# Optimization experiments

Hardware: AMD Instinct MI355X
Metric: run time of the kernel (lower is better)

## Reference

```python
import jax, jax.numpy as jnp
import numpy as np

N = 50000      # nodes
E = 400000     # edges (avg degree 8)
G = 64         # graphs in batch
IN_DIM = 128
OUT_DIM = 16


def _linear_params(key, fan_in, fan_out):
    k1, k2 = jax.random.split(key)
    s = 1.0 / np.sqrt(fan_in)
    W = jax.random.uniform(k1, (fan_in, fan_out), minval=-s, maxval=s, dtype=jnp.float32)
    b = jax.random.uniform(k2, (fan_out,), minval=-s, maxval=s, dtype=jnp.float32)
    return W, b


def setup_inputs() -> dict:
    key = jax.random.key(0)
    ks = jax.random.split(key, 12)
    x = jax.random.normal(ks[0], (N, IN_DIM), dtype=jnp.float32)
    edge_index = jax.random.randint(ks[1], (2, E), 0, N)
    # balanced graph assignment (sorted, every graph id present)
    batch = (jnp.arange(N) * G) // N
    W1, b1 = _linear_params(ks[2], IN_DIM, 64)
    W2, b2 = _linear_params(ks[3], 64, 256)
    W3, b3 = _linear_params(ks[4], 256, 512)
    W4, b4 = _linear_params(ks[5], 512, 64)
    Wr, br = _linear_params(ks[6], IN_DIM, 64)
    fc1_W, fc1_b = _linear_params(ks[7], 64, 64)
    fc2_W, fc2_b = _linear_params(ks[8], 64, OUT_DIM)
    ln_g = jnp.ones((64,), jnp.float32); ln_b = jnp.zeros((64,), jnp.float32)
    fcn_g = jnp.ones((64,), jnp.float32); fcn_b = jnp.zeros((64,), jnp.float32)
    return dict(x=x, edge_index=edge_index, batch=batch,
                W1=W1, b1=b1, W2=W2, b2=b2, W3=W3, b3=b3, W4=W4, b4=b4,
                Wr=Wr, br=br, ln_g=ln_g, ln_b=ln_b,
                fc1_W=fc1_W, fc1_b=fc1_b, fcn_g=fcn_g, fcn_b=fcn_b,
                fc2_W=fc2_W, fc2_b=fc2_b)


def _leaky_relu(h):
    return jnp.where(h >= 0, h, 0.01 * h)


def _layer_norm(h, g, b, eps=1e-5):
    m = jnp.mean(h, axis=-1, keepdims=True)
    v = jnp.var(h, axis=-1, keepdims=True)
    return (h - m) * jax.lax.rsqrt(v + eps) * g + b


def reference(x, edge_index, batch, W1, b1, W2, b2, W3, b3, W4, b4,
              Wr, br, ln_g, ln_b, fc1_W, fc1_b, fcn_g, fcn_b, fc2_W, fc2_b):
    src, dst = edge_index[0], edge_index[1]
    n = x.shape[0]
    # PyG GCNConv normalization with self-loops: deg = 1 + in-degree
    deg = jax.ops.segment_sum(jnp.ones(src.shape[0], x.dtype), dst, num_segments=n) + 1.0
    dis = jax.lax.rsqrt(deg)                 # [N]
    edge_norm = (dis[src] * dis[dst])[:, None]   # [E,1]
    self_norm = (dis * dis)[:, None]             # [N,1]

    def gcn_conv(h, W, b):
        h = h @ W                                            # transform first (PyG order)
        agg = jax.ops.segment_sum(h[src] * edge_norm, dst, num_segments=n)
        return agg + h * self_norm + b                       # self-loop term + bias

    residual = x @ Wr + br
    h = _leaky_relu(gcn_conv(x, W1, b1))
    h = _leaky_relu(gcn_conv(h, W2, b2))
    h = _leaky_relu(gcn_conv(h, W3, b3))
    h = _leaky_relu(gcn_conv(h, W4, b4))
    h = _layer_norm(h + residual, ln_g, ln_b)
    # global max pool over graphs
    p = jax.ops.segment_max(h, batch, num_segments=G)        # [G,64]
    p = _layer_norm(p @ fc1_W + fc1_b, fcn_g, fcn_b)
    p = _leaky_relu(p)
    return p @ fc2_W + fc2_b                                 # [G,16]
```

## Files before the change

kernel.cpp:

```cpp
#include <hip/hip_runtime.h>
#include <hip/hip_bf16.h>
#include <math.h>

typedef short bf16x8 __attribute__((ext_vector_type(8)));
typedef short bf16x4 __attribute__((ext_vector_type(4)));
typedef float f32x4 __attribute__((ext_vector_type(4)));

__device__ inline unsigned short f2bf(float f) {
  unsigned u = __float_as_uint(f);
  u += 0x7FFF + ((u >> 16) & 1);
  return (unsigned short)(u >> 16);
}
__device__ inline float bf2f(unsigned short h) {
  return __uint_as_float(((unsigned)h) << 16);
}


__global__ __launch_bounds__(256) void zero_i32(int* __restrict__ p, int n) {
  int i = blockIdx.x * 256 + threadIdx.x;
  if (i < n) p[i] = 0;
}

__global__ __launch_bounds__(256) void count_k(const int* __restrict__ dst, int* __restrict__ cnt, int e) {
  int i = blockIdx.x * 256 + threadIdx.x;
  if (i < e) atomicAdd(&cnt[dst[i]], 1);
}

__global__ __launch_bounds__(256) void dis_k(const int* __restrict__ cnt, float* __restrict__ dis, int n) {
  int i = blockIdx.x * 256 + threadIdx.x;
  if (i < n) dis[i] = rsqrtf((float)cnt[i] + 1.0f);
}

__global__ __launch_bounds__(256) void scan_a(const int* __restrict__ cnt, int* __restrict__ bsum, int n) {
  int i = blockIdx.x * 256 + threadIdx.x;
  int v = (i < n) ? cnt[i] : 0;
#pragma unroll
  for (int o = 32; o > 0; o >>= 1) v += __shfl_xor(v, o);
  __shared__ int ws[4];
  if ((threadIdx.x & 63) == 0) ws[threadIdx.x >> 6] = v;
  __syncthreads();
  if (threadIdx.x == 0) bsum[blockIdx.x] = ws[0] + ws[1] + ws[2] + ws[3];
}

__global__ __launch_bounds__(256) void scan_b(const int* __restrict__ bsum, int* __restrict__ bpre,
                                              int* __restrict__ off_n, int nb) {
  __shared__ int s[256];
  int t = threadIdx.x;
  int v = (t < nb) ? bsum[t] : 0;
  s[t] = v;
  __syncthreads();
  for (int o = 1; o < 256; o <<= 1) {
    int u = (t >= o) ? s[t - o] : 0;
    __syncthreads();
    s[t] += u;
    __syncthreads();
  }
  if (t < nb) bpre[t] = s[t] - v;
  if (t == 255) off_n[0] = s[255];
}

__global__ __launch_bounds__(256) void scan_c(const int* __restrict__ cnt, const int* __restrict__ bpre,
                                              int* __restrict__ off, int* __restrict__ cursor, int n) {
  __shared__ int s[256];
  int i = blockIdx.x * 256 + threadIdx.x;
  int t = threadIdx.x;
  int v = (i < n) ? cnt[i] : 0;
  s[t] = v;
  __syncthreads();
  for (int o = 1; o < 256; o <<= 1) {
    int u = (t >= o) ? s[t - o] : 0;
    __syncthreads();
    s[t] += u;
    __syncthreads();
  }
  if (i < n) {
    int ov = bpre[blockIdx.x] + s[t] - v;
    off[i] = ov;
    cursor[i] = ov;
  }
}

__global__ __launch_bounds__(256) void scatter_k(const int* __restrict__ src, const int* __restrict__ dst,
                                                 int* __restrict__ cursor, int* __restrict__ csr, int e) {
  int i = blockIdx.x * 256 + threadIdx.x;
  if (i < e) {
    int p = atomicAdd(&cursor[dst[i]], 1);
    csr[p] = src[i];
  }
}


__global__ __launch_bounds__(256) void wconv_k(const float* __restrict__ W1, const float* __restrict__ Wr,
                                               const float* __restrict__ W2, const float* __restrict__ W3,
                                               const float* __restrict__ W4,
                                               short* __restrict__ o1, short* __restrict__ oR,
                                               short* __restrict__ o2, short* __restrict__ o3,
                                               short* __restrict__ o4) {
  int b = blockIdx.x;
  const float* W; short* O; int K, N, nr;
  if (b < 64)       { W = W1; O = o1; K = 128; N = 64;  nr = b; }
  else if (b < 128) { W = Wr; O = oR; K = 128; N = 64;  nr = b - 64; }
  else if (b < 384) { W = W2; O = o2; K = 64;  N = 256; nr = b - 128; }
  else if (b < 896) { W = W3; O = o3; K = 256; N = 512; nr = b - 384; }
  else              { W = W4; O = o4; K = 512; N = 64;  nr = b - 896; }
  for (int k = threadIdx.x; k < K; k += 256)
    O[(size_t)nr * K + k] = (short)f2bf(W[(size_t)k * N + nr]);
}


template<int KT, int NTOT, int WM, int WN, int BIAS, int RELU, int ABF, int OBF, int SPLIT, int SCL, int BLK>
__global__ __launch_bounds__(256, BLK) void mgemm(const void* __restrict__ Av,
                                                  const short* __restrict__ Wc,
                                                  const float* __restrict__ bias,
                                                  void* __restrict__ Cv, void* __restrict__ Cv2,
                                                  const float* __restrict__ scl, int M) {
  __shared__ short As[64 * WM][ABF ? 40 : 72];
  __shared__ short Bs[64 * WN][40];
  const int tid = threadIdx.x;
  const int row0 = blockIdx.x * (64 * WM);
  const int col0 = blockIdx.y * (64 * WN);
  const int w = tid >> 6, lane = tid & 63;
  const int wm = w / WN, wn = w % WN;
  const int rm = wm * 64, cn = wn * 64;
  const int lm = lane & 15, lk = (lane >> 4) * 8;

  f32x4 acc[4][4];
#pragma unroll
  for (int i = 0; i < 4; i++)
#pragma unroll
    for (int j = 0; j < 4; j++)
#pragma unroll
      for (int r = 0; r < 4; r++) acc[i][j][r] = 0.f;

  for (int k0 = 0; k0 < KT; k0 += 32) {
#pragma unroll
    for (int p = 0; p < WM; p++) {
      int r = (tid >> 2) + p * 64;
      int kseg = (tid & 3) * 8;
      int gr = row0 + r;
      if (ABF) {
        bf16x8 v = {0, 0, 0, 0, 0, 0, 0, 0};
        if (gr < M) v = *(const bf16x8*)((const short*)Av + (size_t)gr * KT + k0 + kseg);
        *(bf16x8*)&As[r][kseg] = v;
      } else {
        float4 v0 = {0.f, 0.f, 0.f, 0.f}, v1 = {0.f, 0.f, 0.f, 0.f};
        if (gr < M) {
          const float* ap = (const float*)Av + (size_t)gr * KT + k0 + kseg;
          v0 = *(const float4*)ap;
          v1 = *(const float4*)(ap + 4);
        }
        float vv[8] = {v0.x, v0.y, v0.z, v0.w, v1.x, v1.y, v1.z, v1.w};
        bf16x8 hv, lv;
#pragma unroll
        for (int j = 0; j < 8; j++) {
          unsigned short h = f2bf(vv[j]);
          hv[j] = (short)h;
          lv[j] = (short)f2bf(vv[j] - bf2f(h));
        }
        *(bf16x8*)&As[r][kseg] = hv;
        *(bf16x8*)&As[r][32 + kseg] = lv;
      }
    }
#pragma unroll
    for (int p = 0; p < WN; p++) {
      int nr = (tid >> 2) + p * 64;
      int seg = (tid & 3) * 8;
      *(bf16x8*)&Bs[nr][seg] = *(const bf16x8*)(Wc + (size_t)(col0 + nr) * KT + k0 + seg);
    }
    __syncthreads();

    bf16x8 ah[4], al[4], bb[4];
#pragma unroll
    for (int mt = 0; mt < 4; mt++) {
      ah[mt] = *(const bf16x8*)&As[rm + mt * 16 + lm][lk];
      if (!ABF) al[mt] = *(const bf16x8*)&As[rm + mt * 16 + lm][32 + lk];
    }
#pragma unroll
    for (int nt = 0; nt < 4; nt++) bb[nt] = *(const bf16x8*)&Bs[cn + nt * 16 + lm][lk];
#pragma unroll
    for (int mt = 0; mt < 4; mt++)
#pragma unroll
      for (int nt = 0; nt < 4; nt++) {
        acc[mt][nt] = __builtin_amdgcn_mfma_f32_16x16x32_bf16(ah[mt], bb[nt], acc[mt][nt], 0, 0, 0);
        if (!ABF)
          acc[mt][nt] = __builtin_amdgcn_mfma_f32_16x16x32_bf16(al[mt], bb[nt], acc[mt][nt], 0, 0, 0);
      }
    __syncthreads();
  }

  if (SPLIT) {
    short* epi = (short*)&As[0][0];
    if (wn == 0) {
#pragma unroll
      for (int mt = 0; mt < 4; mt++) {
        int lr = rm + mt * 16 + (lane >> 4) * 4;
#pragma unroll
        for (int r = 0; r < 4; r++) {
          int gr = row0 + lr + r;
          float sc = (SCL && gr < M) ? scl[gr] : 0.f;
#pragma unroll
          for (int nt = 0; nt < 4; nt++)
            epi[(lr + r) * 64 + nt * 16 + lm] = (short)f2bf(acc[mt][nt][r] * sc);
        }
      }
    } else {
#pragma unroll
      for (int mt = 0; mt < 4; mt++) {
        int grb = row0 + rm + mt * 16 + (lane >> 4) * 4;
#pragma unroll
        for (int nt = 0; nt < 4; nt++) {
          int gc = nt * 16 + lm;
          float bv = bias[gc];
#pragma unroll
          for (int r = 0; r < 4; r++) {
            int gr = grb + r;
            if (gr < M) ((float*)Cv2)[(size_t)gr * 64 + gc] = acc[mt][nt][r] + bv;
          }
        }
      }
    }
    __syncthreads();
    int base = tid * 32;
    int row = base >> 6, col = base & 63;
    int gr = row0 + row;
    if (gr < M) {
#pragma unroll
      for (int q = 0; q < 4; q++)
        *(bf16x8*)((short*)Cv + (size_t)gr * 64 + col + q * 8) = *(bf16x8*)&epi[base + q * 8];
    }
  } else if (OBF && WM == 1) {
    short* epi = &Bs[0][0];
    const int NCOL = 64 * WN;
    float bvv[4];
#pragma unroll
    for (int nt = 0; nt < 4; nt++) bvv[nt] = BIAS ? bias[col0 + cn + nt * 16 + lm] : 0.f;
#pragma unroll
    for (int mt = 0; mt < 4; mt++) {
      __syncthreads();
#pragma unroll
      for (int r = 0; r < 4; r++) {
        int gr = row0 + mt * 16 + (lane >> 4) * 4 + r;
        float sc = (SCL && gr < M) ? scl[gr] : 1.f;
#pragma unroll
        for (int nt = 0; nt < 4; nt++) {
          float v = acc[mt][nt][r] + bvv[nt];
          if (RELU) v = (v >= 0.f) ? v : 0.01f * v;
          if (SCL) v *= sc;
          epi[((lane >> 4) * 4 + r) * NCOL + cn + nt * 16 + lm] = (short)f2bf(v);
        }
      }
      __syncthreads();
      const int per = (16 * NCOL) / 256;
      int base = tid * per;
      int lr = base / NCOL, lc = base % NCOL;
      int gr = row0 + mt * 16 + lr;
      if (gr < M) {
#pragma unroll
        for (int q = 0; q < per / 8; q++)
          *(bf16x8*)((short*)Cv + (size_t)gr * NTOT + col0 + lc + q * 8) = *(bf16x8*)&epi[base + q * 8];
      }
    }
  } else {
#pragma unroll
    for (int mt = 0; mt < 4; mt++) {
      int grb = row0 + rm + mt * 16 + (lane >> 4) * 4;
#pragma unroll
      for (int nt = 0; nt < 4; nt++) {
        int gc = col0 + cn + nt * 16 + lm;
        float bv = BIAS ? bias[gc] : 0.f;
#pragma unroll
        for (int r = 0; r < 4; r++) {
          int gr = grb + r;
          if (gr < M) {
            float v = acc[mt][nt][r] + bv;
            if (RELU) v = (v >= 0.f) ? v : 0.01f * v;
            if (SCL) v *= scl[gr];
            if (OBF) ((short*)Cv)[(size_t)gr * NTOT + gc] = (short)f2bf(v);
            else     ((float*)Cv)[(size_t)gr * NTOT + gc] = v;
          }
        }
      }
    }
  }
}


__global__ __launch_bounds__(256, 5) void fused34_k(const short* __restrict__ z3,
                                                    const short* __restrict__ W3c,
                                                    const float* __restrict__ b3,
                                                    const short* __restrict__ W4c,
                                                    const float* __restrict__ dis,
                                                    float* __restrict__ T4, int M) {
  __shared__ short Bs[32][264];
  __shared__ short Hs[64][40];
  __shared__ short Ws4[64][40];
  const int tid = threadIdx.x;
  const int row0 = blockIdx.x * 64;
  const int w = tid >> 6, lane = tid & 63;
  const int lm = lane & 15, lk = (lane >> 4) * 8;
  const int rquad = (lane >> 4) * 4;

  bf16x8 afr[8];
  {
    int gr = row0 + w * 16 + lm;
    bool ok = gr < M;
    const short* zp = z3 + (size_t)gr * 256 + lk;
#pragma unroll
    for (int kc = 0; kc < 8; kc++) {
      bf16x8 v = {0, 0, 0, 0, 0, 0, 0, 0};
      if (ok) v = *(const bf16x8*)(zp + kc * 32);
      afr[kc] = v;
    }
  }

  f32x4 t4acc[4];
#pragma unroll
  for (int nt = 0; nt < 4; nt++)
#pragma unroll
    for (int r = 0; r < 4; r++) t4acc[nt][r] = 0.f;

  for (int c = 0; c < 16; c++) {
#pragma unroll
    for (int q = 0; q < 4; q++) {
      int flat = q * 2048 + tid * 8;
      int rr = flat >> 8, cc = flat & 255;
      *(bf16x8*)&Bs[rr][cc] = *(const bf16x8*)(W3c + (size_t)c * 32 * 256 + flat);
    }
    Ws4[tid >> 2][(tid & 3) * 8 + 0] = 0;
    *(bf16x8*)&Ws4[tid >> 2][(tid & 3) * 8] =
        *(const bf16x8*)(W4c + (size_t)(tid >> 2) * 512 + c * 32 + (tid & 3) * 8);
    __syncthreads();

    f32x4 acc1[2];
#pragma unroll
    for (int nt = 0; nt < 2; nt++)
#pragma unroll
      for (int r = 0; r < 4; r++) acc1[nt][r] = 0.f;
#pragma unroll
    for (int k0 = 0; k0 < 8; k0++) {
      bf16x8 bb[2];
#pragma unroll
      for (int nt = 0; nt < 2; nt++) bb[nt] = *(const bf16x8*)&Bs[nt * 16 + lm][k0 * 32 + lk];
#pragma unroll
      for (int nt = 0; nt < 2; nt++)
        acc1[nt] = __builtin_amdgcn_mfma_f32_16x16x32_bf16(afr[k0], bb[nt], acc1[nt], 0, 0, 0);
    }
#pragma unroll
    for (int nt = 0; nt < 2; nt++) {
      float bv = b3[c * 32 + nt * 16 + lm];
#pragma unroll
      for (int r = 0; r < 4; r++) {
        float v = acc1[nt][r] + bv;
        v = (v >= 0.f) ? v : 0.01f * v;
        Hs[w * 16 + rquad + r][nt * 16 + lm] = (short)f2bf(v);
      }
    }
    {
      bf16x8 ah2 = *(const bf16x8*)&Hs[w * 16 + lm][lk];
      bf16x8 bb2[4];
#pragma unroll
      for (int nt = 0; nt < 4; nt++) bb2[nt] = *(const bf16x8*)&Ws4[nt * 16 + lm][lk];
#pragma unroll
      for (int nt = 0; nt < 4; nt++)
        t4acc[nt] = __builtin_amdgcn_mfma_f32_16x16x32_bf16(ah2, bb2[nt], t4acc[nt], 0, 0, 0);
    }
    __syncthreads();
  }
#pragma unroll
  for (int r = 0; r < 4; r++) {
    int gr = row0 + w * 16 + rquad + r;
    float sc = (gr < M) ? dis[gr] : 0.f;
#pragma unroll
    for (int nt = 0; nt < 4; nt++) {
      int gc = nt * 16 + lm;
      if (gr < M) T4[(size_t)gr * 64 + gc] = t4acc[nt][r] * sc;
    }
  }
}


template<int BR, int OSCL>
__global__ __launch_bounds__(256) void aggb64_k(const short* __restrict__ T, const float* __restrict__ dis,
                                                const int* __restrict__ off, const int* __restrict__ csr,
                                                const float* __restrict__ bias, short* __restrict__ Out, int n) {
  int wid = (blockIdx.x * 256 + threadIdx.x) >> 6;
  int lane = threadIdx.x & 63;
  if (wid >= n) return;
  float di = dis[wid];
  int e0 = off[wid], e1 = off[wid + 1];
  float acc = bf2f((unsigned short)T[(size_t)wid * 64 + lane]);
  int e = e0;
  for (; e + 4 <= e1; e += 4) {
    int j0 = csr[e], j1 = csr[e + 1], j2 = csr[e + 2], j3 = csr[e + 3];
    float v0 = bf2f((unsigned short)T[(size_t)j0 * 64 + lane]);
    float v1 = bf2f((unsigned short)T[(size_t)j1 * 64 + lane]);
    float v2 = bf2f((unsigned short)T[(size_t)j2 * 64 + lane]);
    float v3 = bf2f((unsigned short)T[(size_t)j3 * 64 + lane]);
    acc += (v0 + v1) + (v2 + v3);
  }
  for (; e < e1; e++) acc += bf2f((unsigned short)T[(size_t)csr[e] * 64 + lane]);
  float v = di * acc;
  if (BR) {
    v += bias[lane];
    v = (v >= 0.f) ? v : 0.01f * v;
  }
  if (OSCL) v *= di;
  Out[(size_t)wid * 64 + lane] = (short)f2bf(v);
}

__global__ __launch_bounds__(256) void agg64_ln_k(const float* __restrict__ T, const float* __restrict__ dis,
                                                  const int* __restrict__ off, const int* __restrict__ csr,
                                                  const float* __restrict__ bias, const float* __restrict__ resid,
                                                  const float* __restrict__ g, const float* __restrict__ b,
                                                  float* __restrict__ outh, int n) {
  int wid = (blockIdx.x * 256 + threadIdx.x) >> 6;
  int lane = threadIdx.x & 63;
  if (wid >= n) return;
  float di = dis[wid];
  int e0 = off[wid], e1 = off[wid + 1];
  float acc = T[(size_t)wid * 64 + lane];
  int e = e0;
  for (; e + 4 <= e1; e += 4) {
    int j0 = csr[e], j1 = csr[e + 1], j2 = csr[e + 2], j3 = csr[e + 3];
    float v0 = T[(size_t)j0 * 64 + lane];
    float v1 = T[(size_t)j1 * 64 + lane];
    float v2 = T[(size_t)j2 * 64 + lane];
    float v3 = T[(size_t)j3 * 64 + lane];
    acc += (v0 + v1) + (v2 + v3);
  }
  for (; e < e1; e++) acc += T[(size_t)csr[e] * 64 + lane];
  float v = di * acc + bias[lane];
  v = (v >= 0.f) ? v : 0.01f * v;
  v += resid[(size_t)wid * 64 + lane];
  float s = v, ss = v * v;
#pragma unroll
  for (int o = 32; o > 0; o >>= 1) {
    s += __shfl_xor(s, o);
    ss += __shfl_xor(ss, o);
  }
  float m = s * (1.f / 64.f);
  float var = ss * (1.f / 64.f) - m * m;
  float y = (v - m) * rsqrtf(var + 1e-5f) * g[lane] + b[lane];
  outh[(size_t)wid * 64 + lane] = y;
}

__global__ __launch_bounds__(256) void agg256b_k(const short* __restrict__ T, const float* __restrict__ dis,
                                                 const int* __restrict__ off, const int* __restrict__ csr,
                                                 short* __restrict__ Out, int n) {
  int wid = (blockIdx.x * 256 + threadIdx.x) >> 6;
  int lane = threadIdx.x & 63;
  if (wid >= n) return;
  float di = dis[wid];
  int e0 = off[wid], e1 = off[wid + 1];
  bf16x4 sf = *(const bf16x4*)&T[(size_t)wid * 256 + lane * 4];
  float a0 = bf2f((unsigned short)sf[0]);
  float a1 = bf2f((unsigned short)sf[1]);
  float a2 = bf2f((unsigned short)sf[2]);
  float a3 = bf2f((unsigned short)sf[3]);
  int e = e0;
  for (; e + 4 <= e1; e += 4) {
    int j0 = csr[e], j1 = csr[e + 1], j2 = csr[e + 2], j3 = csr[e + 3];
    bf16x4 t0 = *(const bf16x4*)&T[(size_t)j0 * 256 + lane * 4];
    bf16x4 t1 = *(const bf16x4*)&T[(size_t)j1 * 256 + lane * 4];
    bf16x4 t2 = *(const bf16x4*)&T[(size_t)j2 * 256 + lane * 4];
    bf16x4 t3 = *(const bf16x4*)&T[(size_t)j3 * 256 + lane * 4];
    a0 += (bf2f((unsigned short)t0[0]) + bf2f((unsigned short)t1[0])) +
          (bf2f((unsigned short)t2[0]) + bf2f((unsigned short)t3[0]));
    a1 += (bf2f((unsigned short)t0[1]) + bf2f((unsigned short)t1[1])) +
          (bf2f((unsigned short)t2[1]) + bf2f((unsigned short)t3[1]));
    a2 += (bf2f((unsigned short)t0[2]) + bf2f((unsigned short)t1[2])) +
          (bf2f((unsigned short)t2[2]) + bf2f((unsigned short)t3[2]));
    a3 += (bf2f((unsigned short)t0[3]) + bf2f((unsigned short)t1[3])) +
          (bf2f((unsigned short)t2[3]) + bf2f((unsigned short)t3[3]));
  }
  for (; e < e1; e++) {
    bf16x4 t = *(const bf16x4*)&T[(size_t)csr[e] * 256 + lane * 4];
    a0 += bf2f((unsigned short)t[0]);
    a1 += bf2f((unsigned short)t[1]);
    a2 += bf2f((unsigned short)t[2]);
    a3 += bf2f((unsigned short)t[3]);
  }
  bf16x4 o;
  o[0] = (short)f2bf(di * a0);
  o[1] = (short)f2bf(di * a1);
  o[2] = (short)f2bf(di * a2);
  o[3] = (short)f2bf(di * a3);
  *(bf16x4*)&Out[(size_t)wid * 256 + lane * 4] = o;
}


__global__ __launch_bounds__(256) void pool_k(const float* __restrict__ hn, float* __restrict__ p, int n) {
  const int G = 64;
  int g = blockIdx.x;
  int f = threadIdx.x & 63, c = threadIdx.x >> 6;
  long long s = ((long long)g * n + G - 1) / G;
  long long e = ((long long)(g + 1) * n + G - 1) / G;
  float m = -INFINITY;
  for (long long i = s + c; i < e; i += 4) m = fmaxf(m, hn[(size_t)i * 64 + f]);
  __shared__ float red[4][64];
  red[c][f] = m;
  __syncthreads();
  if (c == 0) {
    m = fmaxf(fmaxf(red[0][f], red[1][f]), fmaxf(red[2][f], red[3][f]));
    p[g * 64 + f] = m;
  }
}


__global__ __launch_bounds__(64) void mlp_k(const float* __restrict__ p, const float* __restrict__ fc1W,
                                            const float* __restrict__ fc1b, const float* __restrict__ fng,
                                            const float* __restrict__ fnb, const float* __restrict__ fc2W,
                                            const float* __restrict__ fc2b, float* __restrict__ out) {
  int g = blockIdx.x;
  int lane = threadIdx.x;
  __shared__ float ps[64], qs[64];
  ps[lane] = p[g * 64 + lane];
  __syncthreads();
  float q = fc1b[lane];
#pragma unroll 8
  for (int k = 0; k < 64; k++) q = fmaf(ps[k], fc1W[k * 64 + lane], q);
  float s = q, ss = q * q;
#pragma unroll
  for (int o = 32; o > 0; o >>= 1) {
    s += __shfl_xor(s, o);
    ss += __shfl_xor(ss, o);
  }
  float m = s * (1.f / 64.f);
  float var = ss * (1.f / 64.f) - m * m;
  float y = (q - m) * rsqrtf(var + 1e-5f) * fng[lane] + fnb[lane];
  y = (y >= 0.f) ? y : 0.01f * y;
  qs[lane] = y;
  __syncthreads();
  if (lane < 16) {
    float o = fc2b[lane];
#pragma unroll 8
    for (int k = 0; k < 64; k++) o = fmaf(qs[k], fc2W[k * 16 + lane], o);
    out[g * 16 + lane] = o;
  }
}


extern "C" void kernel_launch(void* const* d_in, const int* in_sizes, int n_in,
                              void* d_out, int out_size, void* d_ws, size_t ws_size,
                              hipStream_t stream) {
  const float* x   = (const float*)d_in[0];
  const int*   ei  = (const int*)d_in[1];
  const float* W1  = (const float*)d_in[3];
  const float* b1  = (const float*)d_in[4];
  const float* W2  = (const float*)d_in[5];
  const float* b2  = (const float*)d_in[6];
  const float* W3  = (const float*)d_in[7];
  const float* b3  = (const float*)d_in[8];
  const float* W4  = (const float*)d_in[9];
  const float* b4  = (const float*)d_in[10];
  const float* Wr  = (const float*)d_in[11];
  const float* br  = (const float*)d_in[12];
  const float* lng = (const float*)d_in[13];
  const float* lnb = (const float*)d_in[14];
  const float* f1W = (const float*)d_in[15];
  const float* f1b = (const float*)d_in[16];
  const float* fng = (const float*)d_in[17];
  const float* fnb = (const float*)d_in[18];
  const float* f2W = (const float*)d_in[19];
  const float* f2b = (const float*)d_in[20];

  int n = in_sizes[0] / 128;
  int e = in_sizes[1] / 2;
  const int* src = ei;
  const int* dst = ei + e;

  float* arena = (float*)d_ws;
  float* resid = arena;
  short* h2b   = (short*)(arena + (size_t)64 * n);
  float* t4    = arena + (size_t)64 * n;
  short* z3b   = (short*)(arena + (size_t)192 * n);
  float* hn    = arena + (size_t)192 * n;
  short* t1b   = (short*)(arena + (size_t)320 * n);
  short* h1b   = (short*)(arena + (size_t)352 * n);
  short* z2b   = (short*)(arena + (size_t)384 * n);
  float* dis   = arena + (size_t)448 * n;
  int* cnt    = (int*)(dis + n);
  int* off    = cnt + n;
  int* cursor = off + n + 1;
  int* csr    = cursor + n;
  int* bsum   = csr + e;
  int* bpre   = bsum + 256;
  float* pool = (float*)(bpre + 256);
  size_t wq = (((size_t)(pool + 4096)) + 15) & ~(size_t)15;
  short* wc1 = (short*)wq;
  short* wcR = wc1 + 8192;
  short* wc2 = wcR + 8192;
  short* wc3 = wc2 + 16384;
  short* wc4 = wc3 + 131072;
  size_t need = ((char*)(wc4 + 32768) - (char*)d_ws) + 64;
  if (ws_size < need) return;

  int nb_n = (n + 255) / 256;
  int nb_e = (e + 255) / 256;
  int nb_w = (n + 3) / 4;
  int g_wide = (n + 63) / 64;
  int g_fused = (n + 127) / 128;

  wconv_k<<<960, 256, 0, stream>>>(W1, Wr, W2, W3, W4, wc1, wcR, wc2, wc3, wc4);

  zero_i32<<<nb_n, 256, 0, stream>>>(cnt, n);
  count_k<<<nb_e, 256, 0, stream>>>(dst, cnt, e);
  dis_k<<<nb_n, 256, 0, stream>>>(cnt, dis, n);
  scan_a<<<nb_n, 256, 0, stream>>>(cnt, bsum, n);
  scan_b<<<1, 256, 0, stream>>>(bsum, bpre, off + n, nb_n);
  scan_c<<<nb_n, 256, 0, stream>>>(cnt, bpre, off, cursor, n);
  scatter_k<<<nb_e, 256, 0, stream>>>(src, dst, cursor, csr, e);

  mgemm<128, 128, 2, 2, 1, 0, 0, 0, 1, 1, 4><<<dim3(g_fused, 1), 256, 0, stream>>>(x, wc1, br, t1b, resid, dis, n);
  aggb64_k<1, 1><<<nb_w, 256, 0, stream>>>(t1b, dis, off, csr, b1, h1b, n);
  aggb64_k<0, 0><<<nb_w, 256, 0, stream>>>(h1b, dis, off, csr, nullptr, z2b, n);
  mgemm<64, 256, 1, 4, 1, 1, 1, 1, 0, 1, 5><<<dim3(g_wide, 1), 256, 0, stream>>>(z2b, wc2, b2, h2b, nullptr, dis, n);
  agg256b_k<<<nb_w, 256, 0, stream>>>(h2b, dis, off, csr, z3b, n);
  fused34_k<<<g_wide, 256, 0, stream>>>(z3b, wc3, b3, wc4, dis, t4, n);
  agg64_ln_k<<<nb_w, 256, 0, stream>>>(t4, dis, off, csr, b4, resid, lng, lnb, hn, n);
  pool_k<<<64, 256, 0, stream>>>(hn, pool, n);
  mlp_k<<<64, 64, 0, stream>>>(pool, f1W, f1b, fng, fnb, f2W, f2b, (float*)d_out);
}
```

Before: 387.9 us.

## Double-buffer fused34 weights, unroll gathers by 8, fuse small kernels

The fused layer-3/4 kernel now double-buffers its W3/W4 tiles in shared memory. It prefetches the next chunk into registers while computing the current one, which removes one barrier per iteration, and occupancy is lowered to 3 blocks to allow for the larger LDS use. The CSR aggregation kernels gain an 8-way unrolled gather loop to keep more loads in flight. The degree-normalisation kernel is folded into scan_c, and pool and MLP are merged into one kernel, removing two launches. The costs are higher register and LDS pressure and lower occupancy in fused34.

```diff
diff --git a/kernel.cpp b/kernel.cpp
--- a/kernel.cpp
+++ b/kernel.cpp
@@ -24,11 +24,6 @@
 __global__ __launch_bounds__(256) void count_k(const int* __restrict__ dst, int* __restrict__ cnt, int e) {
   int i = blockIdx.x * 256 + threadIdx.x;
   if (i < e) atomicAdd(&cnt[dst[i]], 1);
-}
-
-__global__ __launch_bounds__(256) void dis_k(const int* __restrict__ cnt, float* __restrict__ dis, int n) {
-  int i = blockIdx.x * 256 + threadIdx.x;
-  if (i < n) dis[i] = rsqrtf((float)cnt[i] + 1.0f);
 }
 
 __global__ __launch_bounds__(256) void scan_a(const int* __restrict__ cnt, int* __restrict__ bsum, int n) {
@@ -60,7 +55,8 @@
 }
 
 __global__ __launch_bounds__(256) void scan_c(const int* __restrict__ cnt, const int* __restrict__ bpre,
-                                              int* __restrict__ off, int* __restrict__ cursor, int n) {
+                                              int* __restrict__ off, int* __restrict__ cursor,
+                                              float* __restrict__ dis, int n) {
   __shared__ int s[256];
   int i = blockIdx.x * 256 + threadIdx.x;
   int t = threadIdx.x;
@@ -77,6 +73,7 @@
     int ov = bpre[blockIdx.x] + s[t] - v;
     off[i] = ov;
     cursor[i] = ov;
+    dis[i] = rsqrtf((float)v + 1.0f);
   }
 }
 
@@ -285,20 +282,22 @@
 }
 
 
-__global__ __launch_bounds__(256, 5) void fused34_k(const short* __restrict__ z3,
+__global__ __launch_bounds__(256, 3) void fused34_k(const short* __restrict__ z3,
                                                     const short* __restrict__ W3c,
                                                     const float* __restrict__ b3,
                                                     const short* __restrict__ W4c,
                                                     const float* __restrict__ dis,
                                                     float* __restrict__ T4, int M) {
-  __shared__ short Bs[32][264];
+  __shared__ short Bs[2][32][264];
+  __shared__ short Ws4[2][64][40];
   __shared__ short Hs[64][40];
-  __shared__ short Ws4[64][40];
   const int tid = threadIdx.x;
   const int row0 = blockIdx.x * 64;
   const int w = tid >> 6, lane = tid & 63;
   const int lm = lane & 15, lk = (lane >> 4) * 8;
   const int rquad = (lane >> 4) * 4;
+  const int w3row = tid >> 5, w3seg = (tid & 31) * 8;
+  const int w4row = tid >> 2, w4seg = (tid & 3) * 8;
 
   bf16x8 afr[8];
   {
@@ -319,17 +318,32 @@
 #pragma unroll
     for (int r = 0; r < 4; r++) t4acc[nt][r] = 0.f;
 
+  bf16x8 pw3[4];
+  bf16x8 pw4;
+#pragma unroll
+  for (int q = 0; q < 4; q++) {
+    int flat = q * 2048 + tid * 8;
+    pw3[q] = *(const bf16x8*)(W3c + flat);
+  }
+  pw4 = *(const bf16x8*)(W4c + (size_t)w4row * 512 + w4seg);
+#pragma unroll
+  for (int q = 0; q < 4; q++) {
+    int flat = q * 2048 + tid * 8;
+    *(bf16x8*)&Bs[0][flat >> 8][flat & 255] = pw3[q];
+  }
+  *(bf16x8*)&Ws4[0][w4row][w4seg] = pw4;
+  __syncthreads();
+
   for (int c = 0; c < 16; c++) {
-#pragma unroll
-    for (int q = 0; q < 4; q++) {
-      int flat = q * 2048 + tid * 8;
-      int rr = flat >> 8, cc = flat & 255;
-      *(bf16x8*)&Bs[rr][cc] = *(const bf16x8*)(W3c + (size_t)c * 32 * 256 + flat);
-    }
-    Ws4[tid >> 2][(tid & 3) * 8 + 0] = 0;
-    *(bf16x8*)&Ws4[tid >> 2][(tid & 3) * 8] =
-        *(const bf16x8*)(W4c + (size_t)(tid >> 2) * 512 + c * 32 + (tid & 3) * 8);
-    __syncthreads();
+    int cur = c & 1, nxt = cur ^ 1;
+    if (c < 15) {
+#pragma unroll
+      for (int q = 0; q < 4; q++) {
+        int flat = q * 2048 + tid * 8;
+        pw3[q] = *(const bf16x8*)(W3c + (size_t)(c + 1) * 32 * 256 + flat);
+      }
+      pw4 = *(const bf16x8*)(W4c + (size_t)w4row * 512 + (c + 1) * 32 + w4seg);
+    }
 
     f32x4 acc1[2];
 #pragma unroll
@@ -340,7 +354,7 @@
     for (int k0 = 0; k0 < 8; k0++) {
       bf16x8 bb[2];
 #pragma unroll
-      for (int nt = 0; nt < 2; nt++) bb[nt] = *(const bf16x8*)&Bs[nt * 16 + lm][k0 * 32 + lk];
+      for (int nt = 0; nt < 2; nt++) bb[nt] = *(const bf16x8*)&Bs[cur][nt * 16 + lm][k0 * 32 + lk];
 #pragma unroll
       for (int nt = 0; nt < 2; nt++)
         acc1[nt] = __builtin_amdgcn_mfma_f32_16x16x32_bf16(afr[k0], bb[nt], acc1[nt], 0, 0, 0);
@@ -359,10 +373,18 @@
       bf16x8 ah2 = *(const bf16x8*)&Hs[w * 16 + lm][lk];
       bf16x8 bb2[4];
 #pragma unroll
-      for (int nt = 0; nt < 4; nt++) bb2[nt] = *(const bf16x8*)&Ws4[nt * 16 + lm][lk];
+      for (int nt = 0; nt < 4; nt++) bb2[nt] = *(const bf16x8*)&Ws4[cur][nt * 16 + lm][lk];
 #pragma unroll
       for (int nt = 0; nt < 4; nt++)
         t4acc[nt] = __builtin_amdgcn_mfma_f32_16x16x32_bf16(ah2, bb2[nt], t4acc[nt], 0, 0, 0);
+    }
+    if (c < 15) {
+#pragma unroll
+      for (int q = 0; q < 4; q++) {
+        int flat = q * 2048 + tid * 8;
+        *(bf16x8*)&Bs[nxt][flat >> 8][flat & 255] = pw3[q];
+      }
+      *(bf16x8*)&Ws4[nxt][w4row][w4seg] = pw4;
     }
     __syncthreads();
   }
@@ -390,6 +412,19 @@
   int e0 = off[wid], e1 = off[wid + 1];
   float acc = bf2f((unsigned short)T[(size_t)wid * 64 + lane]);
   int e = e0;
+  for (; e + 8 <= e1; e += 8) {
+    int j0 = csr[e], j1 = csr[e + 1], j2 = csr[e + 2], j3 = csr[e + 3];
+    int j4 = csr[e + 4], j5 = csr[e + 5], j6 = csr[e + 6], j7 = csr[e + 7];
+    float v0 = bf2f((unsigned short)T[(size_t)j0 * 64 + lane]);
+    float v1 = bf2f((unsigned short)T[(size_t)j1 * 64 + lane]);
+    float v2 = bf2f((unsigned short)T[(size_t)j2 * 64 + lane]);
+    float v3 = bf2f((unsigned short)T[(size_t)j3 * 64 + lane]);
+    float v4 = bf2f((unsigned short)T[(size_t)j4 * 64 + lane]);
+    float v5 = bf2f((unsigned short)T[(size_t)j5 * 64 + lane]);
+    float v6 = bf2f((unsigned short)T[(size_t)j6 * 64 + lane]);
+    float v7 = bf2f((unsigned short)T[(size_t)j7 * 64 + lane]);
+    acc += ((v0 + v1) + (v2 + v3)) + ((v4 + v5) + (v6 + v7));
+  }
   for (; e + 4 <= e1; e += 4) {
     int j0 = csr[e], j1 = csr[e + 1], j2 = csr[e + 2], j3 = csr[e + 3];
     float v0 = bf2f((unsigned short)T[(size_t)j0 * 64 + lane]);
@@ -420,6 +455,19 @@
   int e0 = off[wid], e1 = off[wid + 1];
   float acc = T[(size_t)wid * 64 + lane];
   int e = e0;
+  for (; e + 8 <= e1; e += 8) {
+    int j0 = csr[e], j1 = csr[e + 1], j2 = csr[e + 2], j3 = csr[e + 3];
+    int j4 = csr[e + 4], j5 = csr[e + 5], j6 = csr[e + 6], j7 = csr[e + 7];
+    float v0 = T[(size_t)j0 * 64 + lane];
+    float v1 = T[(size_t)j1 * 64 + lane];
+    float v2 = T[(size_t)j2 * 64 + lane];
+    float v3 = T[(size_t)j3 * 64 + lane];
+    float v4 = T[(size_t)j4 * 64 + lane];
+    float v5 = T[(size_t)j5 * 64 + lane];
+    float v6 = T[(size_t)j6 * 64 + lane];
+    float v7 = T[(size_t)j7 * 64 + lane];
+    acc += ((v0 + v1) + (v2 + v3)) + ((v4 + v5) + (v6 + v7));
+  }
   for (; e + 4 <= e1; e += 4) {
     int j0 = csr[e], j1 = csr[e + 1], j2 = csr[e + 2], j3 = csr[e + 3];
     float v0 = T[(size_t)j0 * 64 + lane];
@@ -458,20 +506,29 @@
   float a2 = bf2f((unsigned short)sf[2]);
   float a3 = bf2f((unsigned short)sf[3]);
   int e = e0;
+  for (; e + 8 <= e1; e += 8) {
+    bf16x4 t[8];
+#pragma unroll
+    for (int q = 0; q < 8; q++) t[q] = *(const bf16x4*)&T[(size_t)csr[e + q] * 256 + lane * 4];
+#pragma unroll
+    for (int q = 0; q < 8; q++) {
+      a0 += bf2f((unsigned short)t[q][0]);
+      a1 += bf2f((unsigned short)t[q][1]);
+      a2 += bf2f((unsigned short)t[q][2]);
+      a3 += bf2f((unsigned short)t[q][3]);
+    }
+  }
   for (; e + 4 <= e1; e += 4) {
-    int j0 = csr[e], j1 = csr[e + 1], j2 = csr[e + 2], j3 = csr[e + 3];
-    bf16x4 t0 = *(const bf16x4*)&T[(size_t)j0 * 256 + lane * 4];
-    bf16x4 t1 = *(const bf16x4*)&T[(size_t)j1 * 256 + lane * 4];
-    bf16x4 t2 = *(const bf16x4*)&T[(size_t)j2 * 256 + lane * 4];
-    bf16x4 t3 = *(const bf16x4*)&T[(size_t)j3 * 256 + lane * 4];
-    a0 += (bf2f((unsigned short)t0[0]) + bf2f((unsigned short)t1[0])) +
-          (bf2f((unsigned short)t2[0]) + bf2f((unsigned short)t3[0]));
-    a1 += (bf2f((unsigned short)t0[1]) + bf2f((unsigned short)t1[1])) +
-          (bf2f((unsigned short)t2[1]) + bf2f((unsigned short)t3[1]));
-    a2 += (bf2f((unsigned short)t0[2]) + bf2f((unsigned short)t1[2])) +
-          (bf2f((unsigned short)t2[2]) + bf2f((unsigned short)t3[2]));
-    a3 += (bf2f((unsigned short)t0[3]) + bf2f((unsigned short)t1[3])) +
-          (bf2f((unsigned short)t2[3]) + bf2f((unsigned short)t3[3]));
+    bf16x4 t[4];
+#pragma unroll
+    for (int q = 0; q < 4; q++) t[q] = *(const bf16x4*)&T[(size_t)csr[e + q] * 256 + lane * 4];
+#pragma unroll
+    for (int q = 0; q < 4; q++) {
+      a0 += bf2f((unsigned short)t[q][0]);
+      a1 += bf2f((unsigned short)t[q][1]);
+      a2 += bf2f((unsigned short)t[q][2]);
+      a3 += bf2f((unsigned short)t[q][3]);
+    }
   }
   for (; e < e1; e++) {
     bf16x4 t = *(const bf16x4*)&T[(size_t)csr[e] * 256 + lane * 4];
@@ -489,53 +546,47 @@
 }
 
 
-__global__ __launch_bounds__(256) void pool_k(const float* __restrict__ hn, float* __restrict__ p, int n) {
+__global__ __launch_bounds__(256) void pool_mlp_k(const float* __restrict__ hn,
+                                                  const float* __restrict__ fc1W, const float* __restrict__ fc1b,
+                                                  const float* __restrict__ fng, const float* __restrict__ fnb,
+                                                  const float* __restrict__ fc2W, const float* __restrict__ fc2b,
+                                                  float* __restrict__ out, int n) {
   const int G = 64;
   int g = blockIdx.x;
   int f = threadIdx.x & 63, c = threadIdx.x >> 6;
-  long long s = ((long long)g * n + G - 1) / G;
-  long long e = ((long long)(g + 1) * n + G - 1) / G;
+  long long s0 = ((long long)g * n + G - 1) / G;
+  long long e0 = ((long long)(g + 1) * n + G - 1) / G;
   float m = -INFINITY;
-  for (long long i = s + c; i < e; i += 4) m = fmaxf(m, hn[(size_t)i * 64 + f]);
+  for (long long i = s0 + c; i < e0; i += 4) m = fmaxf(m, hn[(size_t)i * 64 + f]);
   __shared__ float red[4][64];
+  __shared__ float ps[64], qs[64];
   red[c][f] = m;
   __syncthreads();
-  if (c == 0) {
-    m = fmaxf(fmaxf(red[0][f], red[1][f]), fmaxf(red[2][f], red[3][f]));
-    p[g * 64 + f] = m;
-  }
-}
-
-
-__global__ __launch_bounds__(64) void mlp_k(const float* __restrict__ p, const float* __restrict__ fc1W,
-                                            const float* __restrict__ fc1b, const float* __restrict__ fng,
-                                            const float* __restrict__ fnb, const float* __restrict__ fc2W,
-                                            const float* __restrict__ fc2b, float* __restrict__ out) {
-  int g = blockIdx.x;
-  int lane = threadIdx.x;
-  __shared__ float ps[64], qs[64];
-  ps[lane] = p[g * 64 + lane];
+  if (c == 0) ps[f] = fmaxf(fmaxf(red[0][f], red[1][f]), fmaxf(red[2][f], red[3][f]));
   __syncthreads();
-  float q = fc1b[lane];
+  if (threadIdx.x < 64) {
+    int lane = threadIdx.x;
+    float q = fc1b[lane];
 #pragma unroll 8
-  for (int k = 0; k < 64; k++) q = fmaf(ps[k], fc1W[k * 64 + lane], q);
-  float s = q, ss = q * q;
-#pragma unroll
-  for (int o = 32; o > 0; o >>= 1) {
-    s += __shfl_xor(s, o);
-    ss += __shfl_xor(ss, o);
-  }
-  float m = s * (1.f / 64.f);
-  float var = ss * (1.f / 64.f) - m * m;
-  float y = (q - m) * rsqrtf(var + 1e-5f) * fng[lane] + fnb[lane];
-  y = (y >= 0.f) ? y : 0.01f * y;
-  qs[lane] = y;
-  __syncthreads();
-  if (lane < 16) {
-    float o = fc2b[lane];
+    for (int k = 0; k < 64; k++) q = fmaf(ps[k], fc1W[k * 64 + lane], q);
+    float s = q, ss = q * q;
+#pragma unroll
+    for (int o = 32; o > 0; o >>= 1) {
+      s += __shfl_xor(s, o);
+      ss += __shfl_xor(ss, o);
+    }
+    float mm = s * (1.f / 64.f);
+    float var = ss * (1.f / 64.f) - mm * mm;
+    float y = (q - mm) * rsqrtf(var + 1e-5f) * fng[lane] + fnb[lane];
+    y = (y >= 0.f) ? y : 0.01f * y;
+    qs[lane] = y;
+    __builtin_amdgcn_wave_barrier();
+    if (lane < 16) {
+      float o = fc2b[lane];
 #pragma unroll 8
-    for (int k = 0; k < 64; k++) o = fmaf(qs[k], fc2W[k * 16 + lane], o);
-    out[g * 16 + lane] = o;
+      for (int k = 0; k < 64; k++) o = fmaf(qs[k], fc2W[k * 16 + lane], o);
+      out[g * 16 + lane] = o;
+    }
   }
 }
 
@@ -605,10 +656,9 @@
 
   zero_i32<<<nb_n, 256, 0, stream>>>(cnt, n);
   count_k<<<nb_e, 256, 0, stream>>>(dst, cnt, e);
-  dis_k<<<nb_n, 256, 0, stream>>>(cnt, dis, n);
   scan_a<<<nb_n, 256, 0, stream>>>(cnt, bsum, n);
   scan_b<<<1, 256, 0, stream>>>(bsum, bpre, off + n, nb_n);
-  scan_c<<<nb_n, 256, 0, stream>>>(cnt, bpre, off, cursor, n);
+  scan_c<<<nb_n, 256, 0, stream>>>(cnt, bpre, off, cursor, dis, n);
   scatter_k<<<nb_e, 256, 0, stream>>>(src, dst, cursor, csr, e);
 
   mgemm<128, 128, 2, 2, 1, 0, 0, 0, 1, 1, 4><<<dim3(g_fused, 1), 256, 0, stream>>>(x, wc1, br, t1b, resid, dis, n);
@@ -618,6 +668,5 @@
   agg256b_k<<<nb_w, 256, 0, stream>>>(h2b, dis, off, csr, z3b, n);
   fused34_k<<<g_wide, 256, 0, stream>>>(z3b, wc3, b3, wc4, dis, t4, n);
   agg64_ln_k<<<nb_w, 256, 0, stream>>>(t4, dis, off, csr, b4, resid, lng, lnb, hn, n);
-  pool_k<<<64, 256, 0, stream>>>(hn, pool, n);
-  mlp_k<<<64, 64, 0, stream>>>(pool, f1W, f1b, fng, fnb, f2W, f2b, (float*)d_out);
-}
+  pool_mlp_k<<<64, 256, 0, stream>>>(hn, f1W, f1b, fng, fnb, f2W, f2b, (float*)d_out, n);
+}
```

After: 378.5 us. -2.4%, faster.
